# Optimization experiments

Measured on AMD Instinct MI355X. Metric: run time of the kernel, lower is better.

Reference implementation:

```python
import jax, jax.numpy as jnp
import numpy as np

CHAR_SIZE, WORD_SIZE = 200, 100000
EC, EW, HID = 128, 300, 512
H2 = HID // 2
NW, TC = 1024, 16
POS, NER = 48, 16


def lstm_layer(x, Wih, Whh, b, reverse=False):
    """PyTorch-gate-order LSTM. x: [T, ..., D] -> [T, ..., H]."""
    H = Whh.shape[1]
    init = (jnp.zeros(x.shape[1:-1] + (H,), x.dtype),) * 2
    def step(carry, xt):
        h, c = carry
        z = xt @ Wih.T + h @ Whh.T + b
        i, f, g, o = jnp.split(z, 4, axis=-1)
        c = jax.nn.sigmoid(f) * c + jax.nn.sigmoid(i) * jnp.tanh(g)
        h = jax.nn.sigmoid(o) * jnp.tanh(c)
        return (h, c), h
    _, hs = jax.lax.scan(step, init, x, reverse=reverse)
    return hs


def bilstm(x, pf, pb):
    hf = lstm_layer(x, *pf)
    hb = lstm_layer(x, *pb, reverse=True)
    return jnp.concatenate([hf, hb], axis=-1)


def setup_inputs() -> dict:
    key = jax.random.key(0)
    ks = iter(jax.random.split(key, 40))
    def p(shape, s=0.05):
        return jax.random.normal(next(ks), shape, jnp.float32) * s
    d = {}
    d['char_emb'] = p((CHAR_SIZE, EC))
    d['word_emb'] = p((WORD_SIZE, EW))
    for pre, din in (('c', EC), ('w', EW + HID)):
        for sfx in ('f', 'b'):
            d[pre + 'Wih_' + sfx] = p((4 * H2, din))
            d[pre + 'Whh_' + sfx] = p((4 * H2, H2))
            d[pre + 'b_' + sfx] = p((4 * H2,))
    d['aW'] = p((HID, HID)); d['ab'] = p((HID,)); d['aw'] = p((HID,))
    d['hpW'] = p((POS, HID)); d['hpb'] = p((POS,))
    d['hnW'] = p((NER, HID)); d['hnb'] = p((NER,))
    d['word_seq'] = jax.random.randint(next(ks), (NW,), 0, WORD_SIZE)
    d['char_seq'] = jax.random.randint(next(ks), (NW, TC), 0, CHAR_SIZE)
    return d


def reference(char_emb, word_emb,
              cWih_f, cWhh_f, cb_f, cWih_b, cWhh_b, cb_b,
              wWih_f, wWhh_f, wb_f, wWih_b, wWhh_b, wb_b,
              aW, ab, aw, hpW, hpb, hnW, hnb,
              word_seq, char_seq):
    # --- per-word char BiLSTM, batched over all NW words (replaces Python loop) ---
    ce = char_emb[char_seq].transpose(1, 0, 2)              # [TC, NW, EC]
    enc = bilstm(ce, (cWih_f, cWhh_f, cb_f), (cWih_b, cWhh_b, cb_b))  # [TC, NW, HID]
    # --- 'self' attention pooling over char positions ---
    energy = jnp.tanh(enc @ aW.T + ab)                      # [TC, NW, HID]
    alpha = jax.nn.softmax(jnp.einsum('h,tnh->tn', aw, energy), axis=0)
    context = jnp.einsum('tn,tnh->nh', alpha, enc)          # [NW, HID]
    # --- word-level BiLSTM over the sentence (batch 1) ---
    x = jnp.concatenate([word_emb[word_seq], context], axis=1)  # [NW, EW+HID]
    out = bilstm(x, (wWih_f, wWhh_f, wb_f), (wWih_b, wWhh_b, wb_b))  # [NW, HID]
    pos = jax.nn.log_softmax(out @ hpW.T + hpb, axis=1)
    ner = jax.nn.log_softmax(out @ hnW.T + hnb, axis=1)
    return pos, ner
```

## Files before the change

### kernel.cpp

```cpp
#include <hip/hip_runtime.h>
#include <hip/hip_bf16.h>
#include <hip/hip_fp16.h>
#include <math.h>

#define NW 1024
#define TC 16
#define EC 128
#define EW 300
#define HID 512
#define H2 256
#define GATES 1024
#define KC (EC + H2)
#define KW (EW + HID)
#define NPOS 48
#define NNER 16

typedef _Float16 h2v __attribute__((ext_vector_type(2)));
union U32H { unsigned int u; h2v h; float f; };

__device__ __forceinline__ float sigf(float x) { return 1.f / (1.f + expf(-x)); }

__global__ __launch_bounds__(256)
void char_gate_gemm(int s,
    const float* __restrict__ char_emb, const int* __restrict__ char_seq,
    const float* __restrict__ Wih_f, const float* __restrict__ Whh_f,
    const float* __restrict__ Wih_b, const float* __restrict__ Whh_b,
    const float* __restrict__ hbuf,
    float* __restrict__ zbuf)
{
    const int d = blockIdx.z;
    const float* Wih = d ? Wih_b : Wih_f;
    const float* Whh = d ? Whh_b : Whh_f;
    const int t_time = d ? (TC - 1 - s) : s;
    const float* hprev = hbuf + (size_t)((s & 1) * 2 + d) * NW * H2;

    __shared__ float As[16][65];
    __shared__ float Bs[16][65];
    const int tid = threadIdx.x;
    const int tx = tid & 15, ty = tid >> 4;
    const int row0 = blockIdx.x * 64;
    const int col0 = blockIdx.y * 64;
    float acc[4][4] = {};
    for (int kb = 0; kb < KC; kb += 16) {
        #pragma unroll
        for (int q = 0; q < 4; ++q) {
            int idx = tid + q * 256;
            int mm = idx >> 4, kk = idx & 15;
            int k = kb + kk;
            int n = row0 + mm;
            float av;
            if (k < EC) {
                int ci = char_seq[n * TC + t_time];
                av = char_emb[(size_t)ci * EC + k];
            } else {
                av = (s == 0) ? 0.f : hprev[(size_t)n * H2 + (k - EC)];
            }
            As[kk][mm] = av;
            int g = col0 + mm;
            Bs[kk][mm] = (k < EC) ? Wih[(size_t)g * EC + k] : Whh[(size_t)g * H2 + (k - EC)];
        }
        __syncthreads();
        #pragma unroll
        for (int kk = 0; kk < 16; ++kk) {
            float a[4], b[4];
            #pragma unroll
            for (int i = 0; i < 4; ++i) a[i] = As[kk][ty * 4 + i];
            #pragma unroll
            for (int j = 0; j < 4; ++j) b[j] = Bs[kk][tx * 4 + j];
            #pragma unroll
            for (int i = 0; i < 4; ++i)
                #pragma unroll
                for (int j = 0; j < 4; ++j) acc[i][j] += a[i] * b[j];
        }
        __syncthreads();
    }
    float* zo = zbuf + (size_t)d * NW * GATES;
    #pragma unroll
    for (int i = 0; i < 4; ++i)
        #pragma unroll
        for (int j = 0; j < 4; ++j)
            zo[(size_t)(row0 + ty * 4 + i) * GATES + (col0 + tx * 4 + j)] = acc[i][j];
}

__global__ __launch_bounds__(256)
void char_pointwise(int s,
    const float* __restrict__ zbuf,
    const float* __restrict__ b_f, const float* __restrict__ b_b,
    float* __restrict__ hbuf,
    float* __restrict__ cbuf,
    float* __restrict__ enc)
{
    int id = blockIdx.x * blockDim.x + threadIdx.x;
    int d = id >> 18;
    int r = id & ((1 << 18) - 1);
    int n = r >> 8, j = r & (H2 - 1);
    const float* bias = d ? b_b : b_f;
    const float* z = zbuf + ((size_t)d * NW + n) * GATES;
    float zi = z[j]         + bias[j];
    float zf = z[H2 + j]    + bias[H2 + j];
    float zg = z[2*H2 + j]  + bias[2*H2 + j];
    float zo = z[3*H2 + j]  + bias[3*H2 + j];
    float c_old = (s == 0) ? 0.f : cbuf[(size_t)d * NW * H2 + r];
    float c = sigf(zf) * c_old + sigf(zi) * tanhf(zg);
    float h = sigf(zo) * tanhf(c);
    cbuf[(size_t)d * NW * H2 + r] = c;
    hbuf[(size_t)(((s + 1) & 1) * 2 + d) * NW * H2 + r] = h;
    int t_time = d ? (TC - 1 - s) : s;
    enc[((size_t)t_time * NW + n) * HID + d * H2 + j] = h;
}

__global__ __launch_bounds__(256)
void score_gemm(const float* __restrict__ enc, const float* __restrict__ aW,
                const float* __restrict__ ab, const float* __restrict__ aw,
                float* __restrict__ part)
{
    __shared__ float As[16][65];
    __shared__ float Bs[16][65];
    __shared__ float red[64][17];
    const int tid = threadIdx.x;
    const int tx = tid & 15, ty = tid >> 4;
    const int row0 = blockIdx.x * 64;
    const int col0 = blockIdx.y * 64;
    float acc[4][4] = {};
    for (int kb = 0; kb < HID; kb += 16) {
        #pragma unroll
        for (int q = 0; q < 4; ++q) {
            int idx = tid + q * 256;
            int mm = idx >> 4, kk = idx & 15;
            As[kk][mm] = enc[(size_t)(row0 + mm) * HID + kb + kk];
            Bs[kk][mm] = aW[(size_t)(col0 + mm) * HID + kb + kk];
        }
        __syncthreads();
        #pragma unroll
        for (int kk = 0; kk < 16; ++kk) {
            float a[4], b[4];
            #pragma unroll
            for (int i = 0; i < 4; ++i) a[i] = As[kk][ty * 4 + i];
            #pragma unroll
            for (int j = 0; j < 4; ++j) b[j] = Bs[kk][tx * 4 + j];
            #pragma unroll
            for (int i = 0; i < 4; ++i)
                #pragma unroll
                for (int j = 0; j < 4; ++j) acc[i][j] += a[i] * b[j];
        }
        __syncthreads();
    }
    #pragma unroll
    for (int i = 0; i < 4; ++i) {
        float rs = 0.f;
        #pragma unroll
        for (int j = 0; j < 4; ++j) {
            int col = col0 + tx * 4 + j;
            rs += tanhf(acc[i][j] + ab[col]) * aw[col];
        }
        red[ty * 4 + i][tx] = rs;
    }
    __syncthreads();
    if (tid < 64) {
        float v = 0.f;
        #pragma unroll
        for (int x = 0; x < 16; ++x) v += red[tid][x];
        part[(size_t)(row0 + tid) * 8 + blockIdx.y] = v;
    }
}

__global__ void alpha_softmax(const float* __restrict__ part, float* __restrict__ al)
{
    int n = blockIdx.x * blockDim.x + threadIdx.x;
    float sc[TC];
    #pragma unroll
    for (int t = 0; t < TC; ++t) {
        float v = 0.f;
        #pragma unroll
        for (int q = 0; q < 8; ++q) v += part[(size_t)(t * NW + n) * 8 + q];
        sc[t] = v;
    }
    float m = -1e30f;
    #pragma unroll
    for (int t = 0; t < TC; ++t) m = fmaxf(m, sc[t]);
    float ssum = 0.f;
    #pragma unroll
    for (int t = 0; t < TC; ++t) { sc[t] = expf(sc[t] - m); ssum += sc[t]; }
    float inv = 1.f / ssum;
    #pragma unroll
    for (int t = 0; t < TC; ++t) al[t * NW + n] = sc[t] * inv;
}

__global__ void context_kernel(const float* __restrict__ al, const float* __restrict__ enc,
                               float* __restrict__ ctx)
{
    int id = blockIdx.x * blockDim.x + threadIdx.x;
    int n = id >> 9, h = id & (HID - 1);
    float v = 0.f;
    #pragma unroll
    for (int t = 0; t < TC; ++t)
        v += al[t * NW + n] * enc[((size_t)t * NW + n) * HID + h];
    ctx[id] = v;
}

__global__ __launch_bounds__(256)
void word_proj_gemm(const float* __restrict__ word_emb, const int* __restrict__ word_seq,
                    const float* __restrict__ ctx,
                    const float* __restrict__ Wih_f, const float* __restrict__ b_fp,
                    const float* __restrict__ Wih_b, const float* __restrict__ b_bp,
                    float* __restrict__ Gw)
{
    const int d = blockIdx.z;
    const float* W = d ? Wih_b : Wih_f;
    const float* bias = d ? b_bp : b_fp;
    __shared__ float As[16][65];
    __shared__ float Bs[16][65];
    const int tid = threadIdx.x;
    const int tx = tid & 15, ty = tid >> 4;
    const int row0 = blockIdx.x * 64;
    const int col0 = blockIdx.y * 64;
    float acc[4][4] = {};
    for (int kb = 0; kb < KW; kb += 16) {
        #pragma unroll
        for (int q = 0; q < 4; ++q) {
            int idx = tid + q * 256;
            int mm = idx >> 4, kk = idx & 15;
            int k = kb + kk;
            int n = row0 + mm;
            float av = 0.f, bv = 0.f;
            if (k < KW) {
                if (k < EW) av = word_emb[(size_t)word_seq[n] * EW + k];
                else        av = ctx[(size_t)n * HID + (k - EW)];
                bv = W[(size_t)(col0 + mm) * KW + k];
            }
            As[kk][mm] = av;
            Bs[kk][mm] = bv;
        }
        __syncthreads();
        #pragma unroll
        for (int kk = 0; kk < 16; ++kk) {
            float a[4], b[4];
            #pragma unroll
            for (int i = 0; i < 4; ++i) a[i] = As[kk][ty * 4 + i];
            #pragma unroll
            for (int j = 0; j < 4; ++j) b[j] = Bs[kk][tx * 4 + j];
            #pragma unroll
            for (int i = 0; i < 4; ++i)
                #pragma unroll
                for (int j = 0; j < 4; ++j) acc[i][j] += a[i] * b[j];
        }
        __syncthreads();
    }
    float* zo = Gw + (size_t)d * NW * GATES;
    #pragma unroll
    for (int i = 0; i < 4; ++i)
        #pragma unroll
        for (int j = 0; j < 4; ++j) {
            int g = col0 + tx * 4 + j;
            zo[(size_t)(row0 + ty * 4 + i) * GATES + g] = acc[i][j] + bias[g];
        }
}

__global__ __launch_bounds__(256)
void pack_whh(const float* __restrict__ Whh_fw, const float* __restrict__ Whh_bw,
              uint4* __restrict__ wpk)
{
    int id = blockIdx.x * 256 + threadIdx.x;
    int d = id >> 15;
    int rem = id & 32767;
    int row = rem >> 5, q = rem & 31;
    const float* W = d ? Whh_bw : Whh_fw;
    const float* src = W + (size_t)row * H2 + q * 8;
    U32H p0, p1, p2, p3;
    p0.h.x = (_Float16)src[0]; p0.h.y = (_Float16)src[1];
    p1.h.x = (_Float16)src[2]; p1.h.y = (_Float16)src[3];
    p2.h.x = (_Float16)src[4]; p2.h.y = (_Float16)src[5];
    p3.h.x = (_Float16)src[6]; p3.h.y = (_Float16)src[7];
    uint4 v; v.x = p0.u; v.y = p1.u; v.z = p2.u; v.w = p3.u;
    wpk[((size_t)d * 32 + q) * 1024 + row] = v;
}

#define FDOT(hreg, wreg, acc) { U32H _h, _w; _h.u = (hreg); _w.u = (wreg); \
    acc = __builtin_amdgcn_fdot2(_h.h, _w.h, acc, false); }
#define LOADW(q) uint4 A##q = wq[(q) * 1024 + tid]; \
                 uint4 B##q = wq[(q) * 1024 + 512 + tid];
#define PINQ(U) asm volatile("" : "+v"(U.x), "+v"(U.y), "+v"(U.z), "+v"(U.w));
#define PINW(q) PINQ(A##q) PINQ(B##q)
#define DOTQ2(q) { uint4 hh = hp4[q]; \
    FDOT(hh.x, A##q.x, a0) FDOT(hh.y, A##q.y, a1) \
    FDOT(hh.z, A##q.z, a2) FDOT(hh.w, A##q.w, a3) \
    FDOT(hh.x, B##q.x, b0) FDOT(hh.y, B##q.y, b1) \
    FDOT(hh.z, B##q.z, b2) FDOT(hh.w, B##q.w, b3) }

__global__ __launch_bounds__(512, 1)
void word_lstm_dir(const uint4* __restrict__ wpk,
                   const float* __restrict__ Gw,
                   float* __restrict__ wout)
{
    extern __shared__ float smem[];
    uint4* lw4 = (uint4*)smem;
    float* zs = smem + 32 * 1024;
    unsigned int* hpk = (unsigned int*)(zs + GATES);

    const int d = blockIdx.x;
    const int tid = threadIdx.x;
    const float* G = Gw + (size_t)d * NW * GATES;
    const uint4* wq = wpk + (size_t)d * 32 * 1024;

    LOADW(0)  LOADW(1)  LOADW(2)  LOADW(3)  LOADW(4)  LOADW(5)
    LOADW(6)  LOADW(7)  LOADW(8)  LOADW(9)  LOADW(10) LOADW(11)
    LOADW(12) LOADW(13) LOADW(14) LOADW(15) LOADW(16) LOADW(17)
    LOADW(18) LOADW(19) LOADW(20) LOADW(21) LOADW(22) LOADW(23)
    PINW(0)  PINW(1)  PINW(2)  PINW(3)  PINW(4)  PINW(5)
    PINW(6)  PINW(7)  PINW(8)  PINW(9)  PINW(10) PINW(11)
    PINW(12) PINW(13) PINW(14) PINW(15) PINW(16) PINW(17)
    PINW(18) PINW(19) PINW(20) PINW(21) PINW(22) PINW(23)
    #pragma unroll
    for (int s = 0; s < 8; ++s) {
        lw4[s * 512 + tid]       = wq[(24 + s) * 1024 + tid];
        lw4[(8 + s) * 512 + tid] = wq[(24 + s) * 1024 + 512 + tid];
    }
    if (tid < 128) hpk[tid] = 0u;
    float c0 = 0.f, c1 = 0.f;
    __syncthreads();

    const int woff = d * H2;
    float g0 = G[(size_t)(d ? (NW - 1) : 0) * GATES + tid];
    float g1 = G[(size_t)(d ? (NW - 1) : 0) * GATES + 512 + tid];
    for (int t = 0; t < NW; ++t) {
        const int tt = d ? (NW - 1 - t) : t;
        float gn0 = 0.f, gn1 = 0.f;
        if (t + 1 < NW) {
            const int tn = d ? (NW - 2 - t) : (t + 1);
            gn0 = G[(size_t)tn * GATES + tid];
            gn1 = G[(size_t)tn * GATES + 512 + tid];
        }
        float a0 = 0.f, a1 = 0.f, a2 = 0.f, a3 = 0.f;
        float b0 = 0.f, b1 = 0.f, b2 = 0.f, b3 = 0.f;
        const uint4* hp4 = (const uint4*)hpk;
        DOTQ2(0)  DOTQ2(1)  DOTQ2(2)  DOTQ2(3)  DOTQ2(4)  DOTQ2(5)
        DOTQ2(6)  DOTQ2(7)  DOTQ2(8)  DOTQ2(9)  DOTQ2(10) DOTQ2(11)
        DOTQ2(12) DOTQ2(13) DOTQ2(14) DOTQ2(15) DOTQ2(16) DOTQ2(17)
        DOTQ2(18) DOTQ2(19) DOTQ2(20) DOTQ2(21) DOTQ2(22) DOTQ2(23)
        #pragma unroll
        for (int q = 24; q < 32; ++q) {
            uint4 hh = hp4[q];
            uint4 wa = lw4[(q - 24) * 512 + tid];
            uint4 wb = lw4[(q - 16) * 512 + tid];
            FDOT(hh.x, wa.x, a0) FDOT(hh.y, wa.y, a1)
            FDOT(hh.z, wa.z, a2) FDOT(hh.w, wa.w, a3)
            FDOT(hh.x, wb.x, b0) FDOT(hh.y, wb.y, b1)
            FDOT(hh.z, wb.z, b2) FDOT(hh.w, wb.w, b3)
        }
        zs[tid]       = (a0 + a1) + (a2 + a3) + g0;
        zs[512 + tid] = (b0 + b1) + (b2 + b3) + g1;
        __syncthreads();
        if (tid < 128) {
            const int u0 = 2 * tid, u1 = u0 + 1;
            float zi0 = zs[u0],       zi1 = zs[u1];
            float zf0 = zs[256 + u0], zf1 = zs[256 + u1];
            float zg0 = zs[512 + u0], zg1 = zs[512 + u1];
            float zo0 = zs[768 + u0], zo1 = zs[768 + u1];
            c0 = sigf(zf0) * c0 + sigf(zi0) * tanhf(zg0);
            float h0 = sigf(zo0) * tanhf(c0);
            c1 = sigf(zf1) * c1 + sigf(zi1) * tanhf(zg1);
            float h1 = sigf(zo1) * tanhf(c1);
            U32H hp; hp.h.x = (_Float16)h0; hp.h.y = (_Float16)h1;
            hpk[tid] = hp.u;
            float2 hv; hv.x = h0; hv.y = h1;
            *(float2*)&wout[(size_t)tt * HID + woff + u0] = hv;
        }
        g0 = gn0; g1 = gn1;
        __syncthreads();
    }
}

__global__ __launch_bounds__(64)
void heads_kernel(const float* __restrict__ wout,
                  const float* __restrict__ hpW, const float* __restrict__ hpb,
                  const float* __restrict__ hnW, const float* __restrict__ hnb,
                  float* __restrict__ out)
{
    const int n = blockIdx.x;
    const int tid = threadIdx.x;
    __shared__ float v[HID];
    #pragma unroll
    for (int q = 0; q < 8; ++q) v[tid + q * 64] = wout[(size_t)n * HID + tid + q * 64];
    __syncthreads();
    float sc = 0.f;
    if (tid < NPOS) {
        for (int k = 0; k < HID; ++k) sc += v[k] * hpW[(size_t)tid * HID + k];
        sc += hpb[tid];
    } else {
        int cc = tid - NPOS;
        for (int k = 0; k < HID; ++k) sc += v[k] * hnW[(size_t)cc * HID + k];
        sc += hnb[cc];
    }
    __shared__ float ssc[64];
    __shared__ float lsep, lsen;
    ssc[tid] = sc;
    __syncthreads();
    if (tid == 0) {
        float m = -1e30f;
        for (int i = 0; i < NPOS; ++i) m = fmaxf(m, ssc[i]);
        float su = 0.f;
        for (int i = 0; i < NPOS; ++i) su += expf(ssc[i] - m);
        lsep = m + logf(su);
    }
    if (tid == 32) {
        float m = -1e30f;
        for (int i = NPOS; i < 64; ++i) m = fmaxf(m, ssc[i]);
        float su = 0.f;
        for (int i = NPOS; i < 64; ++i) su += expf(ssc[i] - m);
        lsen = m + logf(su);
    }
    __syncthreads();
    if (tid < NPOS) out[(size_t)n * NPOS + tid] = sc - lsep;
    else            out[(size_t)NW * NPOS + (size_t)n * NNER + (tid - NPOS)] = sc - lsen;
}

extern "C" void kernel_launch(void* const* d_in, const int* in_sizes, int n_in,
                              void* d_out, int out_size, void* d_ws, size_t ws_size,
                              hipStream_t stream) {
    const float* char_emb = (const float*)d_in[0];
    const float* word_emb = (const float*)d_in[1];
    const float* cWih_f   = (const float*)d_in[2];
    const float* cWhh_f   = (const float*)d_in[3];
    const float* cb_f     = (const float*)d_in[4];
    const float* cWih_b   = (const float*)d_in[5];
    const float* cWhh_b   = (const float*)d_in[6];
    const float* cb_b     = (const float*)d_in[7];
    const float* wWih_f   = (const float*)d_in[8];
    const float* wWhh_f   = (const float*)d_in[9];
    const float* wb_f     = (const float*)d_in[10];
    const float* wWih_b   = (const float*)d_in[11];
    const float* wWhh_b   = (const float*)d_in[12];
    const float* wb_b     = (const float*)d_in[13];
    const float* aW       = (const float*)d_in[14];
    const float* ab       = (const float*)d_in[15];
    const float* aw       = (const float*)d_in[16];
    const float* hpW      = (const float*)d_in[17];
    const float* hpb      = (const float*)d_in[18];
    const float* hnW      = (const float*)d_in[19];
    const float* hnb      = (const float*)d_in[20];
    const int*   word_seq = (const int*)d_in[21];
    const int*   char_seq = (const int*)d_in[22];
    float* out = (float*)d_out;
    float* ws  = (float*)d_ws;

    const size_t OFF_ENC  = 0;
    const size_t OFF_Z    = OFF_ENC  + (size_t)TC * NW * HID;
    const size_t OFF_CH   = OFF_Z    + (size_t)2 * NW * GATES;
    const size_t OFF_CC   = OFF_CH   + (size_t)4 * NW * H2;
    const size_t OFF_CTX  = OFF_CC   + (size_t)2 * NW * H2;
    const size_t OFF_WOUT = OFF_CTX  + (size_t)NW * HID;
    const size_t OFF_PART = OFF_WOUT + (size_t)NW * HID;
    const size_t OFF_AL   = OFF_PART + (size_t)TC * NW * 8;
    const size_t OFF_WPK  = OFF_AL   + (size_t)TC * NW;

    dim3 gchar(NW / 64, GATES / 64, 2);
    for (int s = 0; s < TC; ++s) {
        char_gate_gemm<<<gchar, 256, 0, stream>>>(s, char_emb, char_seq,
            cWih_f, cWhh_f, cWih_b, cWhh_b, ws + OFF_CH, ws + OFF_Z);
        char_pointwise<<<(2 * NW * H2) / 256, 256, 0, stream>>>(s, ws + OFF_Z,
            cb_f, cb_b, ws + OFF_CH, ws + OFF_CC, ws + OFF_ENC);
    }

    pack_whh<<<(2 * 1024 * 32) / 256, 256, 0, stream>>>(wWhh_f, wWhh_b, (uint4*)(ws + OFF_WPK));

    score_gemm<<<dim3(TC * NW / 64, HID / 64), 256, 0, stream>>>(
        ws + OFF_ENC, aW, ab, aw, ws + OFF_PART);
    alpha_softmax<<<NW / 256, 256, 0, stream>>>(ws + OFF_PART, ws + OFF_AL);
    context_kernel<<<(NW * HID) / 256, 256, 0, stream>>>(ws + OFF_AL, ws + OFF_ENC, ws + OFF_CTX);

    word_proj_gemm<<<dim3(NW / 64, GATES / 64, 2), 256, 0, stream>>>(
        word_emb, word_seq, ws + OFF_CTX, wWih_f, wb_f, wWih_b, wb_b, ws + OFF_Z);

    const int lds_bytes = (32 * 1024 + GATES + 128) * 4;
    hipFuncSetAttribute((const void*)word_lstm_dir,
                        hipFuncAttributeMaxDynamicSharedMemorySize, lds_bytes);
    word_lstm_dir<<<2, 512, lds_bytes, stream>>>(
        (const uint4*)(ws + OFF_WPK), ws + OFF_Z, ws + OFF_WOUT);

    heads_kernel<<<NW, 64, 0, stream>>>(ws + OFF_WOUT, hpW, hpb, hnW, hnb, out);
}
```

Measured before the change: 4.348 ms.

## Stash recurrent weights in AGPRs and stream remaining half from LDS and L2

Restructures where the word-LSTM recurrent weights live. The A half of all 32 weight quads is now kept in accumulation registers via explicit accvgpr writes and reads. The B half is split: 16 quads live in LDS and the other 16 are reloaded from global memory (L2-resident) every timestep. This frees VGPRs and keeps the full A matrix on-chip, at the cost of an accvgpr read per dot and 16 global loads per step on the serial recurrence path.

Measured after the change: 4.073 ms. 1.07x faster.

```diff
diff --git a/kernel.cpp b/kernel.cpp
--- a/kernel.cpp
+++ b/kernel.cpp
@@ -86,9 +86,7 @@
 void char_pointwise(int s,
     const float* __restrict__ zbuf,
     const float* __restrict__ b_f, const float* __restrict__ b_b,
-    float* __restrict__ hbuf,
-    float* __restrict__ cbuf,
-    float* __restrict__ enc)
+    float* __restrict__ hbuf, float* __restrict__ cbuf, float* __restrict__ enc)
 {
     int id = blockIdx.x * blockDim.x + threadIdx.x;
     int d = id >> 18;
@@ -277,17 +275,26 @@
 
 #define FDOT(hreg, wreg, acc) { U32H _h, _w; _h.u = (hreg); _w.u = (wreg); \
     acc = __builtin_amdgcn_fdot2(_h.h, _w.h, acc, false); }
-#define LOADW(q) uint4 A##q = wq[(q) * 1024 + tid]; \
-                 uint4 B##q = wq[(q) * 1024 + 512 + tid];
-#define PINQ(U) asm volatile("" : "+v"(U.x), "+v"(U.y), "+v"(U.z), "+v"(U.w));
-#define PINW(q) PINQ(A##q) PINQ(B##q)
-#define DOTQ2(q) { uint4 hh = hp4[q]; \
-    FDOT(hh.x, A##q.x, a0) FDOT(hh.y, A##q.y, a1) \
-    FDOT(hh.z, A##q.z, a2) FDOT(hh.w, A##q.w, a3) \
-    FDOT(hh.x, B##q.x, b0) FDOT(hh.y, B##q.y, b1) \
-    FDOT(hh.z, B##q.z, b2) FDOT(hh.w, B##q.w, b3) }
-
-__global__ __launch_bounds__(512, 1)
+#define DEFQ(q) unsigned int Aq##q##_0, Aq##q##_1, Aq##q##_2, Aq##q##_3;
+#define STASHQ(q) { uint4 w = wq[(q) * 1024 + tid]; \
+    asm volatile("v_accvgpr_write_b32 %0, %1" : "=a"(Aq##q##_0) : "v"(w.x)); \
+    asm volatile("v_accvgpr_write_b32 %0, %1" : "=a"(Aq##q##_1) : "v"(w.y)); \
+    asm volatile("v_accvgpr_write_b32 %0, %1" : "=a"(Aq##q##_2) : "v"(w.z)); \
+    asm volatile("v_accvgpr_write_b32 %0, %1" : "=a"(Aq##q##_3) : "v"(w.w)); }
+#define DOTAQ(q, hh) { unsigned int t0, t1, t2, t3; \
+    asm volatile("v_accvgpr_read_b32 %0, %1" : "=v"(t0) : "a"(Aq##q##_0)); \
+    asm volatile("v_accvgpr_read_b32 %0, %1" : "=v"(t1) : "a"(Aq##q##_1)); \
+    asm volatile("v_accvgpr_read_b32 %0, %1" : "=v"(t2) : "a"(Aq##q##_2)); \
+    asm volatile("v_accvgpr_read_b32 %0, %1" : "=v"(t3) : "a"(Aq##q##_3)); \
+    FDOT(hh.x, t0, a0) FDOT(hh.y, t1, a1) FDOT(hh.z, t2, a2) FDOT(hh.w, t3, a3) }
+#define STEPQ_L(q) { uint4 hh = hl4[q]; DOTAQ(q, hh) \
+    uint4 wb = lw4[(q) * 512 + tid]; \
+    FDOT(hh.x, wb.x, b0) FDOT(hh.y, wb.y, b1) FDOT(hh.z, wb.z, b2) FDOT(hh.w, wb.w, b3) }
+#define STEPQ_S(q, S) { uint4 hh = hl4[q]; DOTAQ(q, hh) \
+    FDOT(hh.x, S.x, b0) FDOT(hh.y, S.y, b1) FDOT(hh.z, S.z, b2) FDOT(hh.w, S.w, b3) }
+#define LOADS(s) uint4 S##s = sq[(s) * 1024];
+
+__global__ __launch_bounds__(512)
 void word_lstm_dir(const uint4* __restrict__ wpk,
                    const float* __restrict__ Gw,
                    float* __restrict__ wout)
@@ -302,28 +309,30 @@
     const float* G = Gw + (size_t)d * NW * GATES;
     const uint4* wq = wpk + (size_t)d * 32 * 1024;
 
-    LOADW(0)  LOADW(1)  LOADW(2)  LOADW(3)  LOADW(4)  LOADW(5)
-    LOADW(6)  LOADW(7)  LOADW(8)  LOADW(9)  LOADW(10) LOADW(11)
-    LOADW(12) LOADW(13) LOADW(14) LOADW(15) LOADW(16) LOADW(17)
-    LOADW(18) LOADW(19) LOADW(20) LOADW(21) LOADW(22) LOADW(23)
-    PINW(0)  PINW(1)  PINW(2)  PINW(3)  PINW(4)  PINW(5)
-    PINW(6)  PINW(7)  PINW(8)  PINW(9)  PINW(10) PINW(11)
-    PINW(12) PINW(13) PINW(14) PINW(15) PINW(16) PINW(17)
-    PINW(18) PINW(19) PINW(20) PINW(21) PINW(22) PINW(23)
-    #pragma unroll
-    for (int s = 0; s < 8; ++s) {
-        lw4[s * 512 + tid]       = wq[(24 + s) * 1024 + tid];
-        lw4[(8 + s) * 512 + tid] = wq[(24 + s) * 1024 + 512 + tid];
-    }
+    DEFQ(0)  DEFQ(1)  DEFQ(2)  DEFQ(3)  DEFQ(4)  DEFQ(5)  DEFQ(6)  DEFQ(7)
+    DEFQ(8)  DEFQ(9)  DEFQ(10) DEFQ(11) DEFQ(12) DEFQ(13) DEFQ(14) DEFQ(15)
+    DEFQ(16) DEFQ(17) DEFQ(18) DEFQ(19) DEFQ(20) DEFQ(21) DEFQ(22) DEFQ(23)
+    DEFQ(24) DEFQ(25) DEFQ(26) DEFQ(27) DEFQ(28) DEFQ(29) DEFQ(30) DEFQ(31)
+    STASHQ(0)  STASHQ(1)  STASHQ(2)  STASHQ(3)  STASHQ(4)  STASHQ(5)  STASHQ(6)  STASHQ(7)
+    STASHQ(8)  STASHQ(9)  STASHQ(10) STASHQ(11) STASHQ(12) STASHQ(13) STASHQ(14) STASHQ(15)
+    STASHQ(16) STASHQ(17) STASHQ(18) STASHQ(19) STASHQ(20) STASHQ(21) STASHQ(22) STASHQ(23)
+    STASHQ(24) STASHQ(25) STASHQ(26) STASHQ(27) STASHQ(28) STASHQ(29) STASHQ(30) STASHQ(31)
+
+    #pragma unroll
+    for (int s = 0; s < 16; ++s)
+        lw4[s * 512 + tid] = wq[s * 1024 + 512 + tid];
     if (tid < 128) hpk[tid] = 0u;
     float c0 = 0.f, c1 = 0.f;
     __syncthreads();
 
+    const uint4* sq = wq + 16 * 1024 + 512 + tid;
     const int woff = d * H2;
     float g0 = G[(size_t)(d ? (NW - 1) : 0) * GATES + tid];
     float g1 = G[(size_t)(d ? (NW - 1) : 0) * GATES + 512 + tid];
     for (int t = 0; t < NW; ++t) {
         const int tt = d ? (NW - 1 - t) : t;
+        LOADS(0)  LOADS(1)  LOADS(2)  LOADS(3)  LOADS(4)  LOADS(5)  LOADS(6)  LOADS(7)
+        LOADS(8)  LOADS(9)  LOADS(10) LOADS(11) LOADS(12) LOADS(13) LOADS(14) LOADS(15)
         float gn0 = 0.f, gn1 = 0.f;
         if (t + 1 < NW) {
             const int tn = d ? (NW - 2 - t) : (t + 1);
@@ -332,21 +341,15 @@
         }
         float a0 = 0.f, a1 = 0.f, a2 = 0.f, a3 = 0.f;
         float b0 = 0.f, b1 = 0.f, b2 = 0.f, b3 = 0.f;
-        const uint4* hp4 = (const uint4*)hpk;
-        DOTQ2(0)  DOTQ2(1)  DOTQ2(2)  DOTQ2(3)  DOTQ2(4)  DOTQ2(5)
-        DOTQ2(6)  DOTQ2(7)  DOTQ2(8)  DOTQ2(9)  DOTQ2(10) DOTQ2(11)
-        DOTQ2(12) DOTQ2(13) DOTQ2(14) DOTQ2(15) DOTQ2(16) DOTQ2(17)
-        DOTQ2(18) DOTQ2(19) DOTQ2(20) DOTQ2(21) DOTQ2(22) DOTQ2(23)
-        #pragma unroll
-        for (int q = 24; q < 32; ++q) {
-            uint4 hh = hp4[q];
-            uint4 wa = lw4[(q - 24) * 512 + tid];
-            uint4 wb = lw4[(q - 16) * 512 + tid];
-            FDOT(hh.x, wa.x, a0) FDOT(hh.y, wa.y, a1)
-            FDOT(hh.z, wa.z, a2) FDOT(hh.w, wa.w, a3)
-            FDOT(hh.x, wb.x, b0) FDOT(hh.y, wb.y, b1)
-            FDOT(hh.z, wb.z, b2) FDOT(hh.w, wb.w, b3)
-        }
+        const uint4* hl4 = (const uint4*)hpk;
+        STEPQ_L(0)  STEPQ_L(1)  STEPQ_L(2)  STEPQ_L(3)
+        STEPQ_L(4)  STEPQ_L(5)  STEPQ_L(6)  STEPQ_L(7)
+        STEPQ_L(8)  STEPQ_L(9)  STEPQ_L(10) STEPQ_L(11)
+        STEPQ_L(12) STEPQ_L(13) STEPQ_L(14) STEPQ_L(15)
+        STEPQ_S(16, S0)  STEPQ_S(17, S1)  STEPQ_S(18, S2)  STEPQ_S(19, S3)
+        STEPQ_S(20, S4)  STEPQ_S(21, S5)  STEPQ_S(22, S6)  STEPQ_S(23, S7)
+        STEPQ_S(24, S8)  STEPQ_S(25, S9)  STEPQ_S(26, S10) STEPQ_S(27, S11)
+        STEPQ_S(28, S12) STEPQ_S(29, S13) STEPQ_S(30, S14) STEPQ_S(31, S15)
         zs[tid]       = (a0 + a1) + (a2 + a3) + g0;
         zs[512 + tid] = (b0 + b1) + (b2 + b3) + g1;
         __syncthreads();
```
